# Performance work log

Hardware: AMD Instinct MI355X
Metric: run time of the kernel (lower is better)

## Reference

```python
import jax, jax.numpy as jnp
import numpy as np

# ---- hyperparameters (from init_kwargs) ----
B, SEQ, D_MODEL = 2, 2048, 1024
D_STATE, D_CONV, EXPAND, HEAD_DIM, CHUNK = 128, 4, 2, 64, 256
D_INNER = EXPAND * D_MODEL            # 2048
NH = D_INNER // HEAD_DIM              # 32 heads
CONV_DIM = D_INNER + 2 * D_STATE      # 2304
D_IN_PROJ = 2 * D_INNER + 2 * D_STATE + NH  # z, xBC, dt -> 4384
D_FF = 4 * D_MODEL
EPS = 1e-12


def setup_inputs() -> dict:
    key = jax.random.key(0)
    ks = jax.random.split(key, 16)
    s = 0.02
    f32 = jnp.float32
    inp = {
        "x": jax.random.normal(ks[0], (B, SEQ, D_MODEL), f32),
        "time_diff": jax.random.uniform(ks[1], (B, SEQ), f32),
        # TiSSD (Mamba2-style) params
        "W_in": jax.random.normal(ks[2], (D_MODEL, D_IN_PROJ), f32) * s,
        "b_in": jnp.zeros((D_IN_PROJ,), f32),
        "conv_w": jax.random.normal(ks[3], (CONV_DIM, D_CONV), f32) * s,
        "conv_b": jnp.zeros((CONV_DIM,), f32),
        "A_log": jnp.log(jnp.arange(1, NH + 1, dtype=f32)),
        "dt_bias": jnp.full((NH,), -2.0, f32),
        "D": jnp.ones((NH,), f32),
        "time_decay": jnp.full((NH,), -3.0, f32),   # time-aware decay rates
        "rms_w": jnp.ones((D_INNER,), f32),
        "W_out": jax.random.normal(ks[4], (D_INNER, D_MODEL), f32) * s,
        "b_out": jnp.zeros((D_MODEL,), f32),
        # wrapper LayerNorm
        "ln_g": jnp.ones((D_MODEL,), f32),
        "ln_b": jnp.zeros((D_MODEL,), f32),
        # FFN
        "fc1_w": jax.random.normal(ks[5], (D_MODEL, D_FF), f32) * s,
        "fc1_b": jnp.zeros((D_FF,), f32),
        "fc2_w": jax.random.normal(ks[6], (D_FF, D_MODEL), f32) * s,
        "fc2_b": jnp.zeros((D_MODEL,), f32),
        "ln2_g": jnp.ones((D_MODEL,), f32),
        "ln2_b": jnp.zeros((D_MODEL,), f32),
    }
    return inp


def _layer_norm(x, g, b, eps=EPS):
    mu = jnp.mean(x, axis=-1, keepdims=True)
    var = jnp.mean(jnp.square(x - mu), axis=-1, keepdims=True)
    return (x - mu) * jax.lax.rsqrt(var + eps) * g + b


def _hardswish(x):
    return x * jnp.clip(x + 3.0, 0.0, 6.0) * (1.0 / 6.0)


def _tissd_forward(x, time_diff, W_in, b_in, conv_w, conv_b, A_log, dt_bias, D,
                   time_decay, rms_w, W_out, b_out):
    b, l, _ = x.shape
    zxbcdt = x @ W_in + b_in                       # [b,l,D_IN_PROJ]
    z = zxbcdt[..., :D_INNER]
    xBC = zxbcdt[..., D_INNER:D_INNER + CONV_DIM]
    dt_raw = zxbcdt[..., -NH:]

    # causal depthwise conv1d (small fixed kernel -> unrolled shifts)
    xp = jnp.pad(xBC, ((0, 0), (D_CONV - 1, 0), (0, 0)))
    xBC_c = conv_b
    for k in range(D_CONV):
        xBC_c = xBC_c + xp[:, k:k + l, :] * conv_w[:, k]
    xBC_c = jax.nn.silu(xBC_c)

    xs = xBC_c[..., :D_INNER]
    Bm = xBC_c[..., D_INNER:D_INNER + D_STATE]     # [b,l,n]
    Cm = xBC_c[..., -D_STATE:]                     # [b,l,n]

    dt = jax.nn.softplus(dt_raw + dt_bias)         # [b,l,h]
    A = -jnp.exp(A_log)                            # [h]
    # time-aware: extra decay proportional to time gap
    dA = dt * A - jax.nn.softplus(time_decay) * time_diff[..., None]  # [b,l,h]

    xh = xs.reshape(b, l, NH, HEAD_DIM)
    xdt = xh * dt[..., None]                       # [b,l,h,p]

    nc = l // CHUNK
    xc = xdt.reshape(b, nc, CHUNK, NH, HEAD_DIM)
    Bc = Bm.reshape(b, nc, CHUNK, D_STATE)
    Cc = Cm.reshape(b, nc, CHUNK, D_STATE)
    dAc = dA.reshape(b, nc, CHUNK, NH).transpose(0, 3, 1, 2)  # [b,h,c,L]

    A_cum = jnp.cumsum(dAc, axis=-1)               # [b,h,c,L]
    seg = A_cum[..., :, None] - A_cum[..., None, :]
    mask = jnp.tril(jnp.ones((CHUNK, CHUNK), bool))
    Lmat = jnp.where(mask, jnp.exp(jnp.where(mask, seg, 0.0)), 0.0)  # [b,h,c,L,L]

    # intra-chunk (diagonal block) output
    Y_diag = jnp.einsum("bcln,bcsn,bhcls,bcshp->bclhp", Cc, Bc, Lmat, xc)

    # per-chunk final states
    decay_states = jnp.exp(A_cum[..., -1:] - A_cum)  # [b,h,c,L]
    states = jnp.einsum("bcln,bhcl,bclhp->bchpn", Bc, decay_states, xc)
    chunk_decay = jnp.exp(A_cum[..., -1])            # [b,h,c]

    # inter-chunk recurrence over nc chunks
    states_t = states.transpose(1, 0, 2, 3, 4)       # [c,b,h,p,n]
    decay_t = chunk_decay.transpose(2, 0, 1)         # [c,b,h]

    def step(carry, inp):
        s_c, d_c = inp
        new = carry * d_c[..., None, None] + s_c
        return new, carry                            # emit state BEFORE chunk

    init = jnp.zeros((b, NH, HEAD_DIM, D_STATE), x.dtype)
    _, prev_states = jax.lax.scan(step, init, (states_t, decay_t))
    prev_states = prev_states.transpose(1, 0, 2, 3, 4)  # [b,c,h,p,n]

    state_decay = jnp.exp(A_cum)                     # [b,h,c,L]
    Y_off = jnp.einsum("bcln,bchpn,bhcl->bclhp", Cc, prev_states, state_decay)

    Y = (Y_diag + Y_off).reshape(b, l, NH, HEAD_DIM) + D[None, None, :, None] * xh
    y = Y.reshape(b, l, D_INNER)

    # gated RMSNorm
    y = y * jax.nn.silu(z)
    y = y * jax.lax.rsqrt(jnp.mean(jnp.square(y), axis=-1, keepdims=True) + EPS) * rms_w
    return y @ W_out + b_out


def reference(x, time_diff, W_in, b_in, conv_w, conv_b, A_log, dt_bias, D,
              time_decay, rms_w, W_out, b_out, ln_g, ln_b,
              fc1_w, fc1_b, fc2_w, fc2_b, ln2_g, ln2_b):
    hidden = _tissd_forward(x, time_diff, W_in, b_in, conv_w, conv_b, A_log,
                            dt_bias, D, time_decay, rms_w, W_out, b_out)
    # num_layers > 1 -> residual; dropout is identity in eval mode
    h = _layer_norm(hidden + x, ln_g, ln_b)
    # FFN with Hardswish and residual LayerNorm
    hid = _hardswish(h @ fc1_w + fc1_b)
    hid = hid @ fc2_w + fc2_b
    out = _layer_norm(hid + h, ln2_g, ln2_b)
    return (out, time_diff)
```

## Files before the change

### kernel.cpp

```cpp
#include <hip/hip_runtime.h>

#define BATCH 2
#define SEQL 2048
#define DM 1024
#define DSTATE 128
#define HD 64
#define CHUNK 256
#define DI 2048
#define NHEADS 32
#define CONVD 2304
#define DPROJ 4384
#define DFF 4096
#define NC 8
#define ROWS (BATCH*SEQL)

typedef unsigned short ushort_t;
typedef short bf16x8 __attribute__((ext_vector_type(8)));
typedef float f32x4 __attribute__((ext_vector_type(4)));

__device__ __forceinline__ float softplus_f(float v){
    return (v > 20.f) ? v : log1pf(expf(v));
}
__device__ __forceinline__ float silu_f(float v){
    return v / (1.f + expf(-v));
}
__device__ __forceinline__ ushort_t f2b(float v){
    union { float f; unsigned int u; } x; x.f = v;
    unsigned int r = x.u + 0x7fffu + ((x.u >> 16) & 1u);
    return (ushort_t)(r >> 16);
}
__device__ __forceinline__ float b2f(ushort_t v){
    union { unsigned int u; float f; } x; x.u = ((unsigned int)v) << 16;
    return x.f;
}

template<int ACT, int OUT_BF16, int TN, int NS, int DTX>
__global__ __launch_bounds__(256) void mfma_gemm_k(
    const ushort_t* __restrict__ A, const ushort_t* __restrict__ Bt,
    const float* __restrict__ bias, float* __restrict__ Cf,
    ushort_t* __restrict__ Cb, float* __restrict__ dtaux,
    int M, int N, int K, int ldc)
{
    constexpr int NT = (TN == 128) ? 4 : 2;
    constexpr int BROWS = TN / 4;
    __shared__ ushort_t As[128*64];
    __shared__ ushort_t Bs[TN*64];
    int tid = threadIdx.x;
    int lane = tid & 63, wave = tid >> 6;
    int m0 = blockIdx.y * 128, n0 = blockIdx.x * TN;
    int Ks = K / NS;
    int kb = (NS > 1) ? blockIdx.z * Ks : 0;
    int wave_m = (TN==128) ? (wave >> 1)*64 : (wave & 1)*64;
    int wave_n = (TN==128) ? (wave & 1)*64 : (wave >> 1)*32;
    int lrow = lane >> 3;
    int lcol = ((lane & 7) ^ lrow) * 8;
    const ushort_t* Abase = A  + (size_t)(m0 + wave*32    + lrow)*K + lcol + kb;
    const ushort_t* Bbase = Bt + (size_t)(n0 + wave*BROWS + lrow)*K + lcol + kb;
    ushort_t* AsW = &As[(wave*32)*64];
    ushort_t* BsW = &Bs[(wave*BROWS)*64];
    f32x4 acc[4][NT];
    #pragma unroll
    for (int i=0;i<4;i++)
        #pragma unroll
        for (int j=0;j<NT;j++) acc[i][j] = (f32x4){0.f,0.f,0.f,0.f};
    int lm = lane & 15;
    int quad = lane >> 4;
    for (int k0 = 0; k0 < Ks; k0 += 64){
        #pragma unroll
        for (int j = 0; j < 4; j++)
            __builtin_amdgcn_global_load_lds(
                (const __attribute__((address_space(1))) void*)(Abase + (size_t)(j*8)*K + k0),
                (__attribute__((address_space(3))) void*)(AsW + j*8*64), 16, 0, 0);
        #pragma unroll
        for (int j = 0; j < BROWS/8; j++)
            __builtin_amdgcn_global_load_lds(
                (const __attribute__((address_space(1))) void*)(Bbase + (size_t)(j*8)*K + k0),
                (__attribute__((address_space(3))) void*)(BsW + j*8*64), 16, 0, 0);
        __syncthreads();
        #pragma unroll
        for (int kk = 0; kk < 64; kk += 32){
            int cb = kk >> 3;
            bf16x8 af[4], bfr[NT];
            #pragma unroll
            for (int mt=0; mt<4; mt++)
                af[mt] = *(const bf16x8*)&As[(wave_m + mt*16 + lm)*64 + (((cb + quad) ^ (lm & 7))*8)];
            #pragma unroll
            for (int nt=0; nt<NT; nt++)
                bfr[nt] = *(const bf16x8*)&Bs[(wave_n + nt*16 + lm)*64 + (((cb + quad) ^ (lm & 7))*8)];
            #pragma unroll
            for (int mt=0; mt<4; mt++)
                #pragma unroll
                for (int nt=0; nt<NT; nt++)
                    acc[mt][nt] = __builtin_amdgcn_mfma_f32_16x16x32_bf16(af[mt], bfr[nt], acc[mt][nt], 0, 0, 0);
        }
        __syncthreads();
    }
    float* Cfo = Cf + (size_t)((NS > 1) ? blockIdx.z : 0) * (size_t)M * ldc;
    int addb = (NS == 1) || (blockIdx.z == 0);
    int crow0 = m0 + wave_m + quad * 4;
    int ccol0 = n0 + wave_n + lm;
    #pragma unroll
    for (int mt=0; mt<4; mt++){
        #pragma unroll
        for (int nt=0; nt<NT; nt++){
            int col = ccol0 + nt*16;
            if (col < N){
                float bv = addb ? bias[col] : 0.f;
                #pragma unroll
                for (int r=0; r<4; r++){
                    int row = crow0 + mt*16 + r;
                    float v = acc[mt][nt][r] + bv;
                    if (ACT == 1){
                        float t = fminf(fmaxf(v + 3.f, 0.f), 6.f);
                        v = v * t * (1.f/6.f);
                    }
                    if (OUT_BF16){
                        Cb[(size_t)row*ldc + col] = f2b(v);
                        if (DTX && col >= N - NHEADS)
                            dtaux[(size_t)row*NHEADS + (col - (N - NHEADS))] = v;
                    } else {
                        Cfo[(size_t)row*ldc + col] = v;
                    }
                }
            }
        }
    }
}

__global__ __launch_bounds__(256) void prep_in_k(const float* __restrict__ x,
                                                 ushort_t* __restrict__ x_bf,
                                                 const float* __restrict__ W_in,
                                                 ushort_t* __restrict__ WinT){
    __shared__ ushort_t tile[32][33];
    int bid = blockIdx.x;
    if (bid < 16384){
        int idx = bid*256 + threadIdx.x;
        x_bf[idx] = f2b(x[idx]);
        return;
    }
    int id2 = bid - 16384;
    int n0 = (id2 % 140)*32, k0 = (id2 / 140)*32;
    int tx = threadIdx.x & 31, ty = threadIdx.x >> 5;
    #pragma unroll
    for (int i = 0; i < 4; i++){
        int k = k0 + ty + i*8;
        int n = n0 + tx;
        float v = (n < DPROJ) ? W_in[(size_t)k*DPROJ + n] : 0.f;
        tile[ty + i*8][tx] = f2b(v);
    }
    __syncthreads();
    #pragma unroll
    for (int i = 0; i < 4; i++)
        WinT[(size_t)(n0 + ty + i*8)*DM + k0 + tx] = tile[tx][ty + i*8];
}

__global__ __launch_bounds__(256) void transpose3_k(const float* __restrict__ Wout,
                                                    const float* __restrict__ fc1w,
                                                    const float* __restrict__ fc2w,
                                                    ushort_t* __restrict__ WoutT,
                                                    ushort_t* __restrict__ fc1T,
                                                    ushort_t* __restrict__ fc2T){
    __shared__ ushort_t tile[32][33];
    int bid = blockIdx.x;
    const float* W; ushort_t* Wt; int K, N, gx, id;
    if (bid < 2048){        W = Wout; Wt = WoutT; K = DI;  N = DM;  gx = 32;  id = bid; }
    else if (bid < 6144){   W = fc1w; Wt = fc1T;  K = DM;  N = DFF; gx = 128; id = bid - 2048; }
    else {                  W = fc2w; Wt = fc2T;  K = DFF; N = DM;  gx = 32;  id = bid - 6144; }
    int n0 = (id % gx)*32, k0 = (id / gx)*32;
    int tx = threadIdx.x & 31, ty = threadIdx.x >> 5;
    #pragma unroll
    for (int i = 0; i < 4; i++){
        int k = k0 + ty + i*8;
        int n = n0 + tx;
        tile[ty + i*8][tx] = f2b(W[(size_t)k*N + n]);
    }
    __syncthreads();
    #pragma unroll
    for (int i = 0; i < 4; i++)
        Wt[(size_t)(n0 + ty + i*8)*K + k0 + tx] = tile[tx][ty + i*8];
}

__global__ __launch_bounds__(256) void conv_silu_k(const ushort_t* __restrict__ zx,
                                                   const float* __restrict__ conv_w,
                                                   const float* __restrict__ conv_b,
                                                   const float* __restrict__ dt,
                                                   ushort_t* __restrict__ convb,
                                                   float* __restrict__ xdt){
    int idx = blockIdx.x*256 + threadIdx.x;
    int c = idx % CONVD;
    int row = idx / CONVD;
    int t = row & (SEQL-1);
    float acc = conv_b[c];
    #pragma unroll
    for (int k = 0; k < 4; k++){
        int tt = t + k - 3;
        if (tt >= 0)
            acc += b2f(zx[((size_t)(row + k - 3))*DPROJ + DI + c]) * conv_w[c*4 + k];
    }
    float v = silu_f(acc);
    convb[idx] = f2b(v);
    if (c < DI)
        xdt[(size_t)row*DI + c] = v * dt[(size_t)row*NHEADS + (c >> 6)];
}

__global__ __launch_bounds__(256) void dt_scan_k(const float* __restrict__ dtaux,
                                                 const float* __restrict__ time_diff,
                                                 const float* __restrict__ A_log,
                                                 const float* __restrict__ dt_bias,
                                                 const float* __restrict__ time_decay,
                                                 float* __restrict__ dt_out,
                                                 float* __restrict__ Acum){
    __shared__ float s[CHUNK];
    int bid = blockIdx.x;
    int c = bid % NC;
    int h = (bid / NC) % NHEADS;
    int b = bid / (NC*NHEADS);
    int l = threadIdx.x;
    int t = c*CHUNK + l;
    float dtr = dtaux[((size_t)(b*SEQL + t))*NHEADS + h];
    float dtv = softplus_f(dtr + dt_bias[h]);
    float A = -expf(A_log[h]);
    float dA = dtv*A - softplus_f(time_decay[h]) * time_diff[b*SEQL + t];
    dt_out[(size_t)(b*SEQL + t)*NHEADS + h] = dtv;
    s[l] = dA;
    __syncthreads();
    for (int off = 1; off < CHUNK; off <<= 1){
        float v = (l >= off) ? s[l-off] : 0.f;
        __syncthreads();
        s[l] += v;
        __syncthreads();
    }
    Acum[((size_t)(b*NHEADS + h))*SEQL + t] = s[l];
}

__global__ __launch_bounds__(256) void g_mfma_k(const ushort_t* __restrict__ convb,
                                                ushort_t* __restrict__ G){
    __shared__ ushort_t As[64*136];
    __shared__ ushort_t Bs[64*136];
    int bc = blockIdx.z;
    int l0 = blockIdx.y*64, s0 = blockIdx.x*64;
    int tid = threadIdx.x;
    int lane = tid & 63, wave = tid >> 6;
    int lm = lane & 15, quad = lane >> 4;
    const ushort_t* base = convb + (size_t)bc*CHUNK*CONVD;
    #pragma unroll
    for (int i = 0; i < 4; i++){
        int e = tid + i*256;
        int r = e >> 4, k = (e & 15)*8;
        *(bf16x8*)&As[r*136 + k] = *(const bf16x8*)&base[(size_t)(l0+r)*CONVD + DI + DSTATE + k];
        *(bf16x8*)&Bs[r*136 + k] = *(const bf16x8*)&base[(size_t)(s0+r)*CONVD + DI + k];
    }
    __syncthreads();
    f32x4 acc[4];
    #pragma unroll
    for (int j=0;j<4;j++) acc[j] = (f32x4){0.f,0.f,0.f,0.f};
    #pragma unroll
    for (int kk = 0; kk < 4; kk++){
        bf16x8 af = *(const bf16x8*)&As[(wave*16+lm)*136 + kk*32 + quad*8];
        #pragma unroll
        for (int nt = 0; nt < 4; nt++){
            bf16x8 bfr = *(const bf16x8*)&Bs[(nt*16+lm)*136 + kk*32 + quad*8];
            acc[nt] = __builtin_amdgcn_mfma_f32_16x16x32_bf16(af, bfr, acc[nt], 0, 0, 0);
        }
    }
    ushort_t* g = G + (size_t)bc*CHUNK*CHUNK;
    #pragma unroll
    for (int nt = 0; nt < 4; nt++)
        #pragma unroll
        for (int r = 0; r < 4; r++)
            g[(size_t)(l0 + wave*16 + quad*4 + r)*CHUNK + s0 + nt*16 + lm] = f2b(acc[nt][r]);
}

#define RSX 264
#define RSB 72
__global__ __launch_bounds__(256) void states_mfma_k(const ushort_t* __restrict__ convb,
                                                     const float* __restrict__ xdt,
                                                     const float* __restrict__ Acum,
                                                     float* __restrict__ states){
    __shared__ ushort_t xw[64*RSX];
    __shared__ ushort_t Bt[128*RSB];
    __shared__ float Acs[CHUNK];
    int bid = blockIdx.x;
    int h = bid % NHEADS;
    int c = (bid / NHEADS) % NC;
    int b = bid / (NHEADS*NC);
    int tid = threadIdx.x;
    int lane = tid & 63, wave = tid >> 6;
    int lm = lane & 15, quad = lane >> 4;
    Acs[tid] = Acum[((size_t)(b*NHEADS + h))*SEQL + c*CHUNK + tid];
    __syncthreads();
    float AcL = Acs[CHUNK-1];
    {
        const float* xg = xdt + ((size_t)(b*SEQL + c*CHUNK))*DI + h*HD;
        #pragma unroll
        for (int j8 = 0; j8 < 8; j8++){
            int s0 = wave*64 + j8*8;
            bf16x8 pk;
            #pragma unroll
            for (int j = 0; j < 8; j++)
                pk[j] = (short)f2b(expf(AcL - Acs[s0+j]) * xg[(size_t)(s0+j)*DI + lane]);
            *(bf16x8*)&xw[lane*RSX + s0] = pk;
        }
    }
    f32x4 acc[8];
    #pragma unroll
    for (int j=0;j<8;j++) acc[j] = (f32x4){0.f,0.f,0.f,0.f};
    const ushort_t* bbase = convb + ((size_t)(b*SEQL + c*CHUNK))*CONVD + DI;
    for (int l0 = 0; l0 < CHUNK; l0 += 64){
        __syncthreads();
        #pragma unroll
        for (int i = 0; i < 32; i++){
            int e = tid + i*256; int l = e >> 7, n = e & 127;
            Bt[n*RSB + l] = bbase[(size_t)(l0+l)*CONVD + n];
        }
        __syncthreads();
        #pragma unroll
        for (int kk = 0; kk < 2; kk++){
            bf16x8 af = *(const bf16x8*)&xw[(wave*16+lm)*RSX + l0 + kk*32 + quad*8];
            #pragma unroll
            for (int nt = 0; nt < 8; nt++){
                bf16x8 bfr = *(const bf16x8*)&Bt[(nt*16+lm)*RSB + kk*32 + quad*8];
                acc[nt] = __builtin_amdgcn_mfma_f32_16x16x32_bf16(af, bfr, acc[nt], 0, 0, 0);
            }
        }
    }
    float* outp = states + ((size_t)((b*NC + c)*NHEADS + h))*(HD*DSTATE);
    #pragma unroll
    for (int nt = 0; nt < 8; nt++)
        #pragma unroll
        for (int r = 0; r < 4; r++)
            outp[(size_t)(wave*16 + quad*4 + r)*DSTATE + nt*16 + lm] = acc[nt][r];
}

__global__ __launch_bounds__(256) void prev_scan_k(const float* __restrict__ states,
                                                   const float* __restrict__ Acum,
                                                   float* __restrict__ prev){
    int bid = blockIdx.x;
    int h = bid % NHEADS, b = bid / NHEADS;
    int tid = threadIdx.x;
    const float* AcB = Acum + ((size_t)(b*NHEADS + h))*SEQL;
    float dec[NC];
    #pragma unroll
    for (int c = 0; c < NC; c++) dec[c] = expf(AcB[c*CHUNK + CHUNK-1]);
    for (int j = 0; j < 32; j++){
        int e = tid + j*256;
        float carry = 0.f;
        #pragma unroll
        for (int c = 0; c < NC; c++){
            size_t idx = ((size_t)((b*NC + c)*NHEADS + h))*(HD*DSTATE) + e;
            prev[idx] = carry;
            carry = carry*dec[c] + states[idx];
        }
    }
}

#define RLX 264
#define RLP 136
__global__ __launch_bounds__(256) void y_mfma_k(const ushort_t* __restrict__ convb,
                                                const ushort_t* __restrict__ G,
                                                const float* __restrict__ Acum,
                                                const float* __restrict__ prev,
                                                const float* __restrict__ Dp,
                                                const float* __restrict__ xdt,
                                                ushort_t* __restrict__ Ybf){
    __shared__ ushort_t xdtT[64*RLX];
    __shared__ ushort_t prevs[64*RLP];
    __shared__ float Acs[CHUNK];
    int bid = blockIdx.x;
    int h = bid % NHEADS;
    int c = (bid / NHEADS) % NC;
    int b = bid / (NHEADS*NC);
    int tid = threadIdx.x;
    int lane = tid & 63, wave = tid >> 6;
    int lm = lane & 15, quad = lane >> 4;

    Acs[tid] = Acum[((size_t)(b*NHEADS + h))*SEQL + c*CHUNK + tid];
    {
        const float* pv = prev + ((size_t)((b*NC + c)*NHEADS + h))*(HD*DSTATE);
        #pragma unroll
        for (int i = 0; i < 32; i++){
            int e = tid + i*256; int p = e >> 7, n = e & 127;
            prevs[p*RLP + n] = f2b(pv[e]);
        }
    }
    {
        const float* xg = xdt + ((size_t)(b*SEQL + c*CHUNK))*DI + h*HD;
        #pragma unroll
        for (int j8 = 0; j8 < 8; j8++){
            int s0 = wave*64 + j8*8;
            bf16x8 pk;
            #pragma unroll
            for (int j = 0; j < 8; j++)
                pk[j] = (short)f2b(xg[(size_t)(s0+j)*DI + lane]);
            *(bf16x8*)&xdtT[lane*RLX + s0] = pk;
        }
    }
    __syncthreads();

    int   lrow[4];  float Alr[4], eAlr[4];
    #pragma unroll
    for (int mt = 0; mt < 4; mt++){
        lrow[mt] = (mt*4 + wave)*16 + lm;
        Alr[mt]  = Acs[lrow[mt]];
        eAlr[mt] = expf(Alr[mt]);
    }
    const ushort_t* Gbase = G + ((size_t)(b*NC + c))*(CHUNK*CHUNK);

    f32x4 acc[4][4];
    #pragma unroll
    for (int i=0;i<4;i++)
        #pragma unroll
        for (int j=0;j<4;j++) acc[i][j] = (f32x4){0.f,0.f,0.f,0.f};

    for (int ks = 0; ks < 8; ks++){
        bf16x8 bfr[4];
        #pragma unroll
        for (int nt = 0; nt < 4; nt++)
            bfr[nt] = *(const bf16x8*)&xdtT[(nt*16+lm)*RLX + ks*32 + quad*8];
        #pragma unroll
        for (int mt = 0; mt < 4; mt++){
            int rblk = mt*4 + wave;
            int nst = rblk/2 + 1;
            if (ks < nst){
                int sbase = ks*32 + quad*8;
                bf16x8 g8 = *(const bf16x8*)&Gbase[(size_t)lrow[mt]*CHUNK + sbase];
                const float4* A4 = (const float4*)(&Acs[sbase]);
                float4 a0 = A4[0], a1 = A4[1];
                float Al = Alr[mt]; int l = lrow[mt];
                float pv[8];
                pv[0] = (sbase+0 <= l) ? b2f((ushort_t)g8[0])*expf(Al - a0.x) : 0.f;
                pv[1] = (sbase+1 <= l) ? b2f((ushort_t)g8[1])*expf(Al - a0.y) : 0.f;
                pv[2] = (sbase+2 <= l) ? b2f((ushort_t)g8[2])*expf(Al - a0.z) : 0.f;
                pv[3] = (sbase+3 <= l) ? b2f((ushort_t)g8[3])*expf(Al - a0.w) : 0.f;
                pv[4] = (sbase+4 <= l) ? b2f((ushort_t)g8[4])*expf(Al - a1.x) : 0.f;
                pv[5] = (sbase+5 <= l) ? b2f((ushort_t)g8[5])*expf(Al - a1.y) : 0.f;
                pv[6] = (sbase+6 <= l) ? b2f((ushort_t)g8[6])*expf(Al - a1.z) : 0.f;
                pv[7] = (sbase+7 <= l) ? b2f((ushort_t)g8[7])*expf(Al - a1.w) : 0.f;
                bf16x8 af;
                #pragma unroll
                for (int j = 0; j < 8; j++) af[j] = (short)f2b(pv[j]);
                #pragma unroll
                for (int nt = 0; nt < 4; nt++)
                    acc[mt][nt] = __builtin_amdgcn_mfma_f32_16x16x32_bf16(af, bfr[nt], acc[mt][nt], 0, 0, 0);
            }
        }
    }
    for (int kc = 0; kc < 4; kc++){
        bf16x8 bfr[4];
        #pragma unroll
        for (int nt = 0; nt < 4; nt++)
            bfr[nt] = *(const bf16x8*)&prevs[(nt*16+lm)*RLP + kc*32 + quad*8];
        #pragma unroll
        for (int mt = 0; mt < 4; mt++){
            int rowg = b*SEQL + c*CHUNK + lrow[mt];
            bf16x8 c8 = *(const bf16x8*)&convb[(size_t)rowg*CONVD + DI + DSTATE + kc*32 + quad*8];
            float e = eAlr[mt];
            bf16x8 af;
            #pragma unroll
            for (int j = 0; j < 8; j++) af[j] = (short)f2b(e * b2f((ushort_t)c8[j]));
            #pragma unroll
            for (int nt = 0; nt < 4; nt++)
                acc[mt][nt] = __builtin_amdgcn_mfma_f32_16x16x32_bf16(af, bfr[nt], acc[mt][nt], 0, 0, 0);
        }
    }
    float Dv = Dp[h];
    #pragma unroll
    for (int mt = 0; mt < 4; mt++){
        int l0 = (mt*4 + wave)*16 + quad*4;
        #pragma unroll
        for (int nt = 0; nt < 4; nt++){
            int p = nt*16 + lm;
            #pragma unroll
            for (int r = 0; r < 4; r++){
                int rowg = b*SEQL + c*CHUNK + l0 + r;
                float xs = b2f(convb[(size_t)rowg*CONVD + h*HD + p]);
                Ybf[(size_t)rowg*DI + h*HD + p] = f2b(acc[mt][nt][r] + Dv*xs);
            }
        }
    }
}

__global__ __launch_bounds__(256) void gate_rms_k(const ushort_t* __restrict__ Yb,
                                                  const ushort_t* __restrict__ zx,
                                                  const float* __restrict__ rms_w,
                                                  ushort_t* __restrict__ yn){
    __shared__ float red[4];
    __shared__ float scale_s;
    int row = blockIdx.x; int tid = threadIdx.x;
    float v[8]; float ss = 0.f;
    #pragma unroll
    for (int i = 0; i < 8; i++){
        int d = tid + i*256;
        float g = b2f(Yb[(size_t)row*DI + d]) * silu_f(b2f(zx[(size_t)row*DPROJ + d]));
        v[i] = g; ss += g*g;
    }
    #pragma unroll
    for (int off = 32; off > 0; off >>= 1) ss += __shfl_down(ss, off);
    int lane = tid & 63, wid = tid >> 6;
    if (lane == 0) red[wid] = ss;
    __syncthreads();
    if (tid == 0) scale_s = rsqrtf((red[0]+red[1]+red[2]+red[3])*(1.f/DI) + 1e-12f);
    __syncthreads();
    float sc = scale_s;
    #pragma unroll
    for (int i = 0; i < 8; i++){
        int d = tid + i*256;
        yn[(size_t)row*DI + d] = f2b(v[i]*sc*rms_w[d]);
    }
}

__global__ __launch_bounds__(256) void ln_hbf_k(const float* __restrict__ a,
                                                const float* __restrict__ a2,
                                                const float* __restrict__ resid,
                                                const float* __restrict__ g,
                                                const float* __restrict__ bw,
                                                ushort_t* __restrict__ bfout){
    __shared__ float redA[4], redB[4];
    __shared__ float mu_s, rs_s;
    int row = blockIdx.x; int tid = threadIdx.x;
    float u[4]; float s = 0.f, s2 = 0.f;
    #pragma unroll
    for (int i = 0; i < 4; i++){
        int d = tid + i*256;
        float val = a[(size_t)row*DM + d] + a2[(size_t)row*DM + d] + resid[(size_t)row*DM + d];
        u[i] = val; s += val; s2 += val*val;
    }
    #pragma unroll
    for (int off = 32; off > 0; off >>= 1){
        s  += __shfl_down(s,  off);
        s2 += __shfl_down(s2, off);
    }
    int lane = tid & 63, wid = tid >> 6;
    if (lane == 0){ redA[wid] = s; redB[wid] = s2; }
    __syncthreads();
    if (tid == 0){
        float S  = redA[0]+redA[1]+redA[2]+redA[3];
        float S2 = redB[0]+redB[1]+redB[2]+redB[3];
        float mu = S*(1.f/DM);
        float var = S2*(1.f/DM) - mu*mu;
        mu_s = mu; rs_s = rsqrtf(var + 1e-12f);
    }
    __syncthreads();
    float mu = mu_s, rs = rs_s;
    #pragma unroll
    for (int i = 0; i < 4; i++){
        int d = tid + i*256;
        bfout[(size_t)row*DM + d] = f2b((u[i]-mu)*rs*g[d] + bw[d]);
    }
}

__global__ __launch_bounds__(256) void ln_final_k(const float* __restrict__ a,
                                                  const float* __restrict__ a2,
                                                  const ushort_t* __restrict__ residb,
                                                  const float* __restrict__ g,
                                                  const float* __restrict__ bw,
                                                  float* __restrict__ outp,
                                                  const float* __restrict__ td){
    __shared__ float redA[4], redB[4];
    __shared__ float mu_s, rs_s;
    int row = blockIdx.x; int tid = threadIdx.x;
    if (row >= ROWS){
        int idx = (row - ROWS)*256 + tid;
        outp[(size_t)ROWS*DM + idx] = td[idx];
        return;
    }
    float u[4]; float s = 0.f, s2 = 0.f;
    #pragma unroll
    for (int i = 0; i < 4; i++){
        int d = tid + i*256;
        float val = a[(size_t)row*DM + d] + a2[(size_t)row*DM + d] + b2f(residb[(size_t)row*DM + d]);
        u[i] = val; s += val; s2 += val*val;
    }
    #pragma unroll
    for (int off = 32; off > 0; off >>= 1){
        s  += __shfl_down(s,  off);
        s2 += __shfl_down(s2, off);
    }
    int lane = tid & 63, wid = tid >> 6;
    if (lane == 0){ redA[wid] = s; redB[wid] = s2; }
    __syncthreads();
    if (tid == 0){
        float S  = redA[0]+redA[1]+redA[2]+redA[3];
        float S2 = redB[0]+redB[1]+redB[2]+redB[3];
        float mu = S*(1.f/DM);
        float var = S2*(1.f/DM) - mu*mu;
        mu_s = mu; rs_s = rsqrtf(var + 1e-12f);
    }
    __syncthreads();
    float mu = mu_s, rs = rs_s;
    #pragma unroll
    for (int i = 0; i < 4; i++){
        int d = tid + i*256;
        outp[(size_t)row*DM + d] = (u[i]-mu)*rs*g[d] + bw[d];
    }
}

extern "C" void kernel_launch(void* const* d_in, const int* in_sizes, int n_in,
                              void* d_out, int out_size, void* d_ws, size_t ws_size,
                              hipStream_t stream){
    const float* x         = (const float*)d_in[0];
    const float* time_diff = (const float*)d_in[1];
    const float* W_in      = (const float*)d_in[2];
    const float* b_in      = (const float*)d_in[3];
    const float* conv_w    = (const float*)d_in[4];
    const float* conv_b    = (const float*)d_in[5];
    const float* A_log     = (const float*)d_in[6];
    const float* dt_bias   = (const float*)d_in[7];
    const float* Dp        = (const float*)d_in[8];
    const float* time_dec  = (const float*)d_in[9];
    const float* rms_w     = (const float*)d_in[10];
    const float* W_out     = (const float*)d_in[11];
    const float* b_out     = (const float*)d_in[12];
    const float* ln_g      = (const float*)d_in[13];
    const float* ln_b      = (const float*)d_in[14];
    const float* fc1_w     = (const float*)d_in[15];
    const float* fc1_b     = (const float*)d_in[16];
    const float* fc2_w     = (const float*)d_in[17];
    const float* fc2_b     = (const float*)d_in[18];
    const float* ln2_g     = (const float*)d_in[19];
    const float* ln2_b     = (const float*)d_in[20];

    float* ws = (float*)d_ws;
    float* zx    = ws;
    float* convb = zx    + 17956864;
    float* dt    = convb + 9437184;
    float* Acum  = dt    + 131072;
    float* xdt   = Acum  + 131072;
    float* r5    = xdt   + 8388608;
    float* ybreg = r5    + 9437184;
    ushort_t* zx_bf  = (ushort_t*)zx;
    float*    dtaux  = zx + 10600000;
    ushort_t* mid_bf = (ushort_t*)zx;
    ushort_t* h_bf   = (ushort_t*)(zx + 8388608);
    ushort_t* convb_bf = (ushort_t*)convb;
    float* outPa  = convb;
    ushort_t* x_bf  = (ushort_t*)xdt;
    ushort_t* WinT  = (ushort_t*)(xdt + 2097152);
    ushort_t* WoutT = (ushort_t*)(xdt + 4194304);
    float* fc2Pa = xdt;
    ushort_t* Gb   = (ushort_t*)r5;
    float* stat = r5 + 1048576;
    float* prev = stat + 4194304;
    ushort_t* yn_bf = (ushort_t*)r5;
    ushort_t* fc1T  = (ushort_t*)(r5 + 4194304);
    ushort_t* fc2T  = (ushort_t*)(r5 + 6291456);
    ushort_t* Ybf = (ushort_t*)ybreg;
    float* outp   = (float*)d_out;

    prep_in_k<<<16384 + 4480, 256, 0, stream>>>(x, x_bf, W_in, WinT);
    mfma_gemm_k<0,1,128,1,1><<<dim3(35, ROWS/128), 256, 0, stream>>>(x_bf, WinT, b_in, nullptr, zx_bf, dtaux, ROWS, DPROJ, DM, DPROJ);
    dt_scan_k<<<BATCH*NHEADS*NC, 256, 0, stream>>>(dtaux, time_diff, A_log, dt_bias, time_dec, dt, Acum);
    conv_silu_k<<<ROWS*CONVD/256, 256, 0, stream>>>(zx_bf, conv_w, conv_b, dt, convb_bf, xdt);
    g_mfma_k<<<dim3(4,4,BATCH*NC), 256, 0, stream>>>(convb_bf, Gb);
    states_mfma_k<<<BATCH*NC*NHEADS, 256, 0, stream>>>(convb_bf, xdt, Acum, stat);
    prev_scan_k<<<BATCH*NHEADS, 256, 0, stream>>>(stat, Acum, prev);
    y_mfma_k<<<BATCH*NC*NHEADS, 256, 0, stream>>>(convb_bf, Gb, Acum, prev, Dp, xdt, Ybf);
    gate_rms_k<<<ROWS, 256, 0, stream>>>(Ybf, zx_bf, rms_w, yn_bf);
    transpose3_k<<<10240, 256, 0, stream>>>(W_out, fc1_w, fc2_w, WoutT, fc1T, fc2T);
    mfma_gemm_k<0,0,64,2,0><<<dim3(DM/64, ROWS/128, 2), 256, 0, stream>>>(yn_bf, WoutT, b_out, outPa, nullptr, nullptr, ROWS, DM, DI, DM);
    ln_hbf_k<<<ROWS, 256, 0, stream>>>(outPa, outPa + (size_t)ROWS*DM, x, ln_g, ln_b, h_bf);
    mfma_gemm_k<1,1,128,1,0><<<dim3(DFF/128, ROWS/128), 256, 0, stream>>>(h_bf, fc1T, fc1_b, nullptr, mid_bf, nullptr, ROWS, DFF, DM, DFF);
    mfma_gemm_k<0,0,64,2,0><<<dim3(DM/64, ROWS/128, 2), 256, 0, stream>>>(mid_bf, fc2T, fc2_b, fc2Pa, nullptr, nullptr, ROWS, DM, DFF, DM);
    ln_final_k<<<ROWS + ROWS/256, 256, 0, stream>>>(fc2Pa, fc2Pa + (size_t)ROWS*DM, h_bf, ln2_g, ln2_b, outp, time_diff);
}
```

Measured before the change: 504.9 us.

## Merge conv and dt-scan kernels, drop xdt buffer, parallelize prev scan

```diff
diff --git a/kernel.cpp b/kernel.cpp
--- a/kernel.cpp
+++ b/kernel.cpp
@@ -180,48 +180,46 @@
         Wt[(size_t)(n0 + ty + i*8)*K + k0 + tx] = tile[tx][ty + i*8];
 }
 
-__global__ __launch_bounds__(256) void conv_silu_k(const ushort_t* __restrict__ zx,
-                                                   const float* __restrict__ conv_w,
-                                                   const float* __restrict__ conv_b,
-                                                   const float* __restrict__ dt,
-                                                   ushort_t* __restrict__ convb,
-                                                   float* __restrict__ xdt){
-    int idx = blockIdx.x*256 + threadIdx.x;
-    int c = idx % CONVD;
-    int row = idx / CONVD;
-    int t = row & (SEQL-1);
-    float acc = conv_b[c];
-    #pragma unroll
-    for (int k = 0; k < 4; k++){
-        int tt = t + k - 3;
-        if (tt >= 0)
-            acc += b2f(zx[((size_t)(row + k - 3))*DPROJ + DI + c]) * conv_w[c*4 + k];
-    }
-    float v = silu_f(acc);
-    convb[idx] = f2b(v);
-    if (c < DI)
-        xdt[(size_t)row*DI + c] = v * dt[(size_t)row*NHEADS + (c >> 6)];
-}
-
-__global__ __launch_bounds__(256) void dt_scan_k(const float* __restrict__ dtaux,
+#define CONVBLKS (ROWS*CONVD/256)
+__global__ __launch_bounds__(256) void conv_dt_k(const ushort_t* __restrict__ zx,
+                                                 const float* __restrict__ conv_w,
+                                                 const float* __restrict__ conv_b,
+                                                 ushort_t* __restrict__ convb,
+                                                 const float* __restrict__ dtaux,
                                                  const float* __restrict__ time_diff,
                                                  const float* __restrict__ A_log,
                                                  const float* __restrict__ dt_bias,
                                                  const float* __restrict__ time_decay,
-                                                 float* __restrict__ dt_out,
+                                                 float* __restrict__ dtH,
                                                  float* __restrict__ Acum){
     __shared__ float s[CHUNK];
     int bid = blockIdx.x;
-    int c = bid % NC;
-    int h = (bid / NC) % NHEADS;
-    int b = bid / (NC*NHEADS);
+    if (bid < CONVBLKS){
+        int idx = bid*256 + threadIdx.x;
+        int c = idx % CONVD;
+        int row = idx / CONVD;
+        int t = row & (SEQL-1);
+        float acc = conv_b[c];
+        #pragma unroll
+        for (int k = 0; k < 4; k++){
+            int tt = t + k - 3;
+            if (tt >= 0)
+                acc += b2f(zx[((size_t)(row + k - 3))*DPROJ + DI + c]) * conv_w[c*4 + k];
+        }
+        convb[idx] = f2b(silu_f(acc));
+        return;
+    }
+    int id2 = bid - CONVBLKS;
+    int c = id2 % NC;
+    int h = (id2 / NC) % NHEADS;
+    int b = id2 / (NC*NHEADS);
     int l = threadIdx.x;
     int t = c*CHUNK + l;
     float dtr = dtaux[((size_t)(b*SEQL + t))*NHEADS + h];
     float dtv = softplus_f(dtr + dt_bias[h]);
     float A = -expf(A_log[h]);
     float dA = dtv*A - softplus_f(time_decay[h]) * time_diff[b*SEQL + t];
-    dt_out[(size_t)(b*SEQL + t)*NHEADS + h] = dtv;
+    dtH[((size_t)(b*NHEADS + h))*SEQL + t] = dtv;
     s[l] = dA;
     __syncthreads();
     for (int off = 1; off < CHUNK; off <<= 1){
@@ -274,12 +272,13 @@
 #define RSX 264
 #define RSB 72
 __global__ __launch_bounds__(256) void states_mfma_k(const ushort_t* __restrict__ convb,
-                                                     const float* __restrict__ xdt,
+                                                     const float* __restrict__ dtH,
                                                      const float* __restrict__ Acum,
                                                      float* __restrict__ states){
     __shared__ ushort_t xw[64*RSX];
     __shared__ ushort_t Bt[128*RSB];
     __shared__ float Acs[CHUNK];
+    __shared__ float dts[CHUNK];
     int bid = blockIdx.x;
     int h = bid % NHEADS;
     int c = (bid / NHEADS) % NC;
@@ -288,17 +287,20 @@
     int lane = tid & 63, wave = tid >> 6;
     int lm = lane & 15, quad = lane >> 4;
     Acs[tid] = Acum[((size_t)(b*NHEADS + h))*SEQL + c*CHUNK + tid];
+    dts[tid] = dtH[((size_t)(b*NHEADS + h))*SEQL + c*CHUNK + tid];
     __syncthreads();
     float AcL = Acs[CHUNK-1];
     {
-        const float* xg = xdt + ((size_t)(b*SEQL + c*CHUNK))*DI + h*HD;
+        const ushort_t* xg = convb + ((size_t)(b*SEQL + c*CHUNK))*CONVD + h*HD;
         #pragma unroll
         for (int j8 = 0; j8 < 8; j8++){
             int s0 = wave*64 + j8*8;
             bf16x8 pk;
             #pragma unroll
-            for (int j = 0; j < 8; j++)
-                pk[j] = (short)f2b(expf(AcL - Acs[s0+j]) * xg[(size_t)(s0+j)*DI + lane]);
+            for (int j = 0; j < 8; j++){
+                int l = s0 + j;
+                pk[j] = (short)f2b(expf(AcL - Acs[l]) * dts[l] * b2f(xg[(size_t)l*CONVD + lane]));
+            }
             *(bf16x8*)&xw[lane*RSX + s0] = pk;
         }
     }
@@ -336,14 +338,17 @@
                                                    const float* __restrict__ Acum,
                                                    float* __restrict__ prev){
     int bid = blockIdx.x;
-    int h = bid % NHEADS, b = bid / NHEADS;
+    int part = bid & 15;
+    int h = (bid >> 4) & (NHEADS-1);
+    int b = bid >> 9;
     int tid = threadIdx.x;
     const float* AcB = Acum + ((size_t)(b*NHEADS + h))*SEQL;
     float dec[NC];
     #pragma unroll
     for (int c = 0; c < NC; c++) dec[c] = expf(AcB[c*CHUNK + CHUNK-1]);
-    for (int j = 0; j < 32; j++){
-        int e = tid + j*256;
+    #pragma unroll
+    for (int j = 0; j < 2; j++){
+        int e = part*512 + j*256 + tid;
         float carry = 0.f;
         #pragma unroll
         for (int c = 0; c < NC; c++){
@@ -359,13 +364,14 @@
 __global__ __launch_bounds__(256) void y_mfma_k(const ushort_t* __restrict__ convb,
                                                 const ushort_t* __restrict__ G,
                                                 const float* __restrict__ Acum,
+                                                const float* __restrict__ dtH,
                                                 const float* __restrict__ prev,
                                                 const float* __restrict__ Dp,
-                                                const float* __restrict__ xdt,
                                                 ushort_t* __restrict__ Ybf){
     __shared__ ushort_t xdtT[64*RLX];
     __shared__ ushort_t prevs[64*RLP];
     __shared__ float Acs[CHUNK];
+    __shared__ float dts[CHUNK];
     int bid = blockIdx.x;
     int h = bid % NHEADS;
     int c = (bid / NHEADS) % NC;
@@ -375,6 +381,7 @@
     int lm = lane & 15, quad = lane >> 4;
 
     Acs[tid] = Acum[((size_t)(b*NHEADS + h))*SEQL + c*CHUNK + tid];
+    dts[tid] = dtH[((size_t)(b*NHEADS + h))*SEQL + c*CHUNK + tid];
     {
         const float* pv = prev + ((size_t)((b*NC + c)*NHEADS + h))*(HD*DSTATE);
         #pragma unroll
@@ -383,15 +390,18 @@
             prevs[p*RLP + n] = f2b(pv[e]);
         }
     }
+    __syncthreads();
     {
-        const float* xg = xdt + ((size_t)(b*SEQL + c*CHUNK))*DI + h*HD;
+        const ushort_t* xg = convb + ((size_t)(b*SEQL + c*CHUNK))*CONVD + h*HD;
         #pragma unroll
         for (int j8 = 0; j8 < 8; j8++){
             int s0 = wave*64 + j8*8;
             bf16x8 pk;
             #pragma unroll
-            for (int j = 0; j < 8; j++)
-                pk[j] = (short)f2b(xg[(size_t)(s0+j)*DI + lane]);
+            for (int j = 0; j < 8; j++){
+                int l = s0 + j;
+                pk[j] = (short)f2b(b2f(xg[(size_t)l*CONVD + lane]) * dts[l]);
+            }
             *(bf16x8*)&xdtT[lane*RLX + s0] = pk;
         }
     }
@@ -623,10 +633,10 @@
     float* ws = (float*)d_ws;
     float* zx    = ws;
     float* convb = zx    + 17956864;
-    float* dt    = convb + 9437184;
-    float* Acum  = dt    + 131072;
-    float* xdt   = Acum  + 131072;
-    float* r5    = xdt   + 8388608;
+    float* dtH   = convb + 9437184;
+    float* Acum  = dtH   + 131072;
+    float* r4    = Acum  + 131072;
+    float* r5    = r4    + 8388608;
     float* ybreg = r5    + 9437184;
     ushort_t* zx_bf  = (ushort_t*)zx;
     float*    dtaux  = zx + 10600000;
@@ -634,10 +644,10 @@
     ushort_t* h_bf   = (ushort_t*)(zx + 8388608);
     ushort_t* convb_bf = (ushort_t*)convb;
     float* outPa  = convb;
-    ushort_t* x_bf  = (ushort_t*)xdt;
-    ushort_t* WinT  = (ushort_t*)(xdt + 2097152);
-    ushort_t* WoutT = (ushort_t*)(xdt + 4194304);
-    float* fc2Pa = xdt;
+    ushort_t* x_bf  = (ushort_t*)r4;
+    ushort_t* WinT  = (ushort_t*)(r4 + 2097152);
+    ushort_t* WoutT = (ushort_t*)(r4 + 4194304);
+    float* fc2Pa = r4;
     ushort_t* Gb   = (ushort_t*)r5;
     float* stat = r5 + 1048576;
     float* prev = stat + 4194304;
@@ -649,12 +659,12 @@
 
     prep_in_k<<<16384 + 4480, 256, 0, stream>>>(x, x_bf, W_in, WinT);
     mfma_gemm_k<0,1,128,1,1><<<dim3(35, ROWS/128), 256, 0, stream>>>(x_bf, WinT, b_in, nullptr, zx_bf, dtaux, ROWS, DPROJ, DM, DPROJ);
-    dt_scan_k<<<BATCH*NHEADS*NC, 256, 0, stream>>>(dtaux, time_diff, A_log, dt_bias, time_dec, dt, Acum);
-    conv_silu_k<<<ROWS*CONVD/256, 256, 0, stream>>>(zx_bf, conv_w, conv_b, dt, convb_bf, xdt);
+    conv_dt_k<<<CONVBLKS + BATCH*NHEADS*NC, 256, 0, stream>>>(zx_bf, conv_w, conv_b, convb_bf,
+                                                              dtaux, time_diff, A_log, dt_bias, time_dec, dtH, Acum);
     g_mfma_k<<<dim3(4,4,BATCH*NC), 256, 0, stream>>>(convb_bf, Gb);
-    states_mfma_k<<<BATCH*NC*NHEADS, 256, 0, stream>>>(convb_bf, xdt, Acum, stat);
-    prev_scan_k<<<BATCH*NHEADS, 256, 0, stream>>>(stat, Acum, prev);
-    y_mfma_k<<<BATCH*NC*NHEADS, 256, 0, stream>>>(convb_bf, Gb, Acum, prev, Dp, xdt, Ybf);
+    states_mfma_k<<<BATCH*NC*NHEADS, 256, 0, stream>>>(convb_bf, dtH, Acum, stat);
+    prev_scan_k<<<BATCH*NHEADS*16, 256, 0, stream>>>(stat, Acum, prev);
+    y_mfma_k<<<BATCH*NC*NHEADS, 256, 0, stream>>>(convb_bf, Gb, Acum, dtH, prev, Dp, Ybf);
     gate_rms_k<<<ROWS, 256, 0, stream>>>(Ybf, zx_bf, rms_w, yn_bf);
     transpose3_k<<<10240, 256, 0, stream>>>(W_out, fc1_w, fc2_w, WoutT, fc1T, fc2T);
     mfma_gemm_k<0,0,64,2,0><<<dim3(DM/64, ROWS/128, 2), 256, 0, stream>>>(yn_bf, WoutT, b_out, outPa, nullptr, nullptr, ROWS, DM, DI, DM);
```

Result: faster. 492.6 us (-2.4%).
